# Kernel optimization log

Hardware: AMD Instinct MI355X
Metric: run time of the kernel (lower is better)

Reference implementation:

```python
import jax, jax.numpy as jnp
import numpy as np

EPS = 1e-12  # tf.math.l2_normalize epsilon guard

def _l2_normalize(x, axis):
    sq = jnp.sum(x * x, axis=axis, keepdims=True)
    return x * jax.lax.rsqrt(jnp.maximum(sq, EPS))

def setup_inputs() -> dict:
    key = jax.random.key(0)
    k1, k2 = jax.random.split(key)
    a = jax.random.normal(k1, (16, 4096, 256), dtype=jnp.float32)
    b = jax.random.normal(k2, (16, 4096, 256), dtype=jnp.float32)
    return {"a": a, "b": b}

def reference(a, b):
    # Original: Dot(axes=[2,2], normalize=True) -> [B,N,N] cosine matrix,
    # then diag_part -> [B,N]. Diagonal entry (i) is cosine(a[:,i,:], b[:,i,:]),
    # so compute only the matching-row cosine similarity.
    a_hat = _l2_normalize(a, axis=2)
    b_hat = _l2_normalize(b, axis=2)
    return jnp.sum(a_hat * b_hat, axis=2)  # [B, N]
```

## Files before the change

kernel.cpp:

```cpp
#include <hip/hip_runtime.h>
#include <math.h>


#define EPS 1e-12f

typedef float f4 __attribute__((ext_vector_type(4)));

__global__ __launch_bounds__(256) void cosine_rows_kernel(
    const f4* __restrict__ a4,
    const f4* __restrict__ b4,
    float* __restrict__ out,
    int nrows)
{
    const int lane = threadIdx.x & 63;
    const int wid  = (blockIdx.x << 2) + (threadIdx.x >> 6);
    const int nw   = gridDim.x << 2;

    for (int base = wid * 4; base < nrows; base += nw * 4) {
        const int i0 = (base + 0) * 64 + lane;
        const int i1 = (base + 1) * 64 + lane;
        const int i2 = (base + 2) * 64 + lane;
        const int i3 = (base + 3) * 64 + lane;
        f4 av0 = a4[i0];
        f4 av1 = a4[i1];
        f4 av2 = a4[i2];
        f4 av3 = a4[i3];
        f4 bv0 = b4[i0];
        f4 bv1 = b4[i1];
        f4 bv2 = b4[i2];
        f4 bv3 = b4[i3];

        f4 avs[4] = {av0, av1, av2, av3};
        f4 bvs[4] = {bv0, bv1, bv2, bv3};

        #pragma unroll
        for (int r = 0; r < 4; ++r) {
            const f4 av = avs[r];
            const f4 bv = bvs[r];
            float saa = av.x * av.x + av.y * av.y + av.z * av.z + av.w * av.w;
            float sbb = bv.x * bv.x + bv.y * bv.y + bv.z * bv.z + bv.w * bv.w;
            float sab = av.x * bv.x + av.y * bv.y + av.z * bv.z + av.w * bv.w;

            #pragma unroll
            for (int off = 32; off > 0; off >>= 1) {
                saa += __shfl_xor(saa, off, 64);
                sbb += __shfl_xor(sbb, off, 64);
                sab += __shfl_xor(sab, off, 64);
            }

            if (lane == 0) {
                const float denom = sqrtf(fmaxf(saa, EPS)) * sqrtf(fmaxf(sbb, EPS));
                out[base + r] = sab / denom;
            }
        }
    }
}

extern "C" void kernel_launch(void* const* d_in, const int* in_sizes, int n_in,
                              void* d_out, int out_size, void* d_ws, size_t ws_size,
                              hipStream_t stream) {
    const float* a = (const float*)d_in[0];
    const float* b = (const float*)d_in[1];
    float* out = (float*)d_out;

    const int nrows = out_size;
    const int blocks = 2048;

    cosine_rows_kernel<<<blocks, 256, 0, stream>>>(
        (const f4*)a, (const f4*)b, out, nrows);
}
```

Before: 142.0 us.

## Assign eight lanes per row with contiguous chunks and nontemporal loads

Each wavefront now handles 8 rows at once. Each group of 8 lanes reads a contiguous 32-float slice of one row and accumulates it serially, so the cross-lane reduction needs 3 shuffle steps instead of 6 per row. Loads use nontemporal hints, since the data is streamed once. The trade-off is a strided per-lane access pattern (each lane reads 128 contiguous bytes), which may coalesce less well than the previous fully contiguous wavefront loads.

```diff
diff --git a/kernel.cpp b/kernel.cpp
--- a/kernel.cpp
+++ b/kernel.cpp
@@ -7,51 +7,42 @@
 typedef float f4 __attribute__((ext_vector_type(4)));
 
 __global__ __launch_bounds__(256) void cosine_rows_kernel(
-    const f4* __restrict__ a4,
-    const f4* __restrict__ b4,
+    const float* __restrict__ a,
+    const float* __restrict__ b,
     float* __restrict__ out,
     int nrows)
 {
     const int lane = threadIdx.x & 63;
     const int wid  = (blockIdx.x << 2) + (threadIdx.x >> 6);
     const int nw   = gridDim.x << 2;
+    const int sub  = lane & 7;
+    const int rloc = lane >> 3;
 
-    for (int base = wid * 4; base < nrows; base += nw * 4) {
-        const int i0 = (base + 0) * 64 + lane;
-        const int i1 = (base + 1) * 64 + lane;
-        const int i2 = (base + 2) * 64 + lane;
-        const int i3 = (base + 3) * 64 + lane;
-        f4 av0 = a4[i0];
-        f4 av1 = a4[i1];
-        f4 av2 = a4[i2];
-        f4 av3 = a4[i3];
-        f4 bv0 = b4[i0];
-        f4 bv1 = b4[i1];
-        f4 bv2 = b4[i2];
-        f4 bv3 = b4[i3];
+    for (int base = wid * 8; base < nrows; base += nw * 8) {
+        const int row = base + rloc;
+        const f4* ap = (const f4*)(a + (size_t)row * 256 + sub * 32);
+        const f4* bp = (const f4*)(b + (size_t)row * 256 + sub * 32);
 
-        f4 avs[4] = {av0, av1, av2, av3};
-        f4 bvs[4] = {bv0, bv1, bv2, bv3};
+        float saa = 0.f, sbb = 0.f, sab = 0.f;
+        #pragma unroll
+        for (int j = 0; j < 8; ++j) {
+            f4 av = __builtin_nontemporal_load(&ap[j]);
+            f4 bv = __builtin_nontemporal_load(&bp[j]);
+            saa += av.x * av.x + av.y * av.y + av.z * av.z + av.w * av.w;
+            sbb += bv.x * bv.x + bv.y * bv.y + bv.z * bv.z + bv.w * bv.w;
+            sab += av.x * bv.x + av.y * bv.y + av.z * bv.z + av.w * bv.w;
+        }
 
         #pragma unroll
-        for (int r = 0; r < 4; ++r) {
-            const f4 av = avs[r];
-            const f4 bv = bvs[r];
-            float saa = av.x * av.x + av.y * av.y + av.z * av.z + av.w * av.w;
-            float sbb = bv.x * bv.x + bv.y * bv.y + bv.z * bv.z + bv.w * bv.w;
-            float sab = av.x * bv.x + av.y * bv.y + av.z * bv.z + av.w * bv.w;
+        for (int off = 4; off > 0; off >>= 1) {
+            saa += __shfl_xor(saa, off, 64);
+            sbb += __shfl_xor(sbb, off, 64);
+            sab += __shfl_xor(sab, off, 64);
+        }
 
-            #pragma unroll
-            for (int off = 32; off > 0; off >>= 1) {
-                saa += __shfl_xor(saa, off, 64);
-                sbb += __shfl_xor(sbb, off, 64);
-                sab += __shfl_xor(sab, off, 64);
-            }
-
-            if (lane == 0) {
-                const float denom = sqrtf(fmaxf(saa, EPS)) * sqrtf(fmaxf(sbb, EPS));
-                out[base + r] = sab / denom;
-            }
+        if (sub == 0) {
+            const float denom = sqrtf(fmaxf(saa, EPS)) * sqrtf(fmaxf(sbb, EPS));
+            out[row] = sab / denom;
         }
     }
 }
@@ -66,6 +57,5 @@
     const int nrows = out_size;
     const int blocks = 2048;
 
-    cosine_rows_kernel<<<blocks, 256, 0, stream>>>(
-        (const f4*)a, (const f4*)b, out, nrows);
+    cosine_rows_kernel<<<blocks, 256, 0, stream>>>(a, b, out, nrows);
 }
```

After: 180.2 us. +26.9%, slower.
